# Performance work log

Hardware: AMD Instinct MI355X
Metric: run time of the kernel (lower is better)

The kernel has to match this reference:

```python
import jax, jax.numpy as jnp
import numpy as np

H, W, D = 160, 160, 16
VOXEL_SIZE = 0.4
VOL_MIN = np.array([-32.0, -32.0, -1.0], dtype=np.float32)
SCALE_MULTIPLIER = 3.0
N_GAUSS = 8192
CHUNK = 64


def setup_inputs() -> dict:
    key = jax.random.key(0)
    k1, k2, k3, k4, k5 = jax.random.split(key, 5)
    vol_min = jnp.asarray(VOL_MIN)
    vol_ext = jnp.array([64.0, 64.0, 6.4], dtype=jnp.float32)
    means3d = jax.random.uniform(k1, (N_GAUSS, 3), jnp.float32) * vol_ext + vol_min
    opacities = jax.random.uniform(k2, (N_GAUSS, 1), jnp.float32)
    # per-axis std devs: 0.2..0.8 m so 3-sigma footprint spans a handful of voxels
    scales = 0.2 + 0.6 * jax.random.uniform(k3, (N_GAUSS, 3), jnp.float32)
    rotations = jax.random.normal(k4, (N_GAUSS, 4), jnp.float32)
    features = jax.random.normal(k5, (N_GAUSS, 32), jnp.float32)
    return {"means3d": means3d, "opacities": opacities, "scales": scales,
            "rotations": rotations, "features": features}


def quat_to_rotmat(q):
    # q: [N,4] wxyz, normalized
    w, x, y, z = q[:, 0], q[:, 1], q[:, 2], q[:, 3]
    R = jnp.stack([
        jnp.stack([1 - 2 * (y * y + z * z), 2 * (x * y - w * z), 2 * (x * z + w * y)], -1),
        jnp.stack([2 * (x * y + w * z), 1 - 2 * (x * x + z * z), 2 * (y * z - w * x)], -1),
        jnp.stack([2 * (x * z - w * y), 2 * (y * z + w * x), 1 - 2 * (x * x + y * y)], -1),
    ], axis=-2)  # [N,3,3]
    return R


def _grid_coords():
    ii, jj, kk = jnp.meshgrid(jnp.arange(H), jnp.arange(W), jnp.arange(D), indexing="ij")
    idx = jnp.stack([ii, jj, kk], axis=-1).astype(jnp.float32)
    return (idx + 0.5) * VOXEL_SIZE + jnp.asarray(VOL_MIN)  # [H,W,D,3] voxel centers


def reference(means3d, opacities, scales, rotations, features):
    x = _grid_coords().reshape(-1, 3)  # [V,3]
    q = rotations / jnp.linalg.norm(rotations, axis=-1, keepdims=True)
    R = quat_to_rotmat(q)
    # covariance = R diag(s^2) R^T
    cov = jnp.einsum("nij,nj,nkj->nik", R, scales * scales, R)
    cov_inv = jnp.linalg.inv(cov)
    sigma = jnp.sqrt(jnp.diagonal(cov, axis1=1, axis2=2))  # [N,3]
    opac = opacities[:, 0]  # [N]
    n = means3d.shape[0]
    nchunks = n // CHUNK

    def chunked(a):
        return a.reshape(nchunks, CHUNK, *a.shape[1:])

    def step(acc, c):
        mu, op, sg, ci, ft = c
        diff = x[:, None, :] - mu[None, :, :]  # [V,CHUNK,3]
        maha = jnp.einsum("vci,cij,vcj->vc", diff, ci, diff)
        # local aggregation cutoff: within scale_multiplier * sigma box around mean
        mask = jnp.all(jnp.abs(diff) <= SCALE_MULTIPLIER * sg[None, :, :], axis=-1)
        w = op[None, :] * jnp.exp(-0.5 * maha) * mask  # [V,CHUNK]
        return acc + w @ ft, None

    acc0 = jnp.zeros((x.shape[0], features.shape[-1]), jnp.float32)
    xs = (chunked(means3d), chunked(opac), chunked(sigma), chunked(cov_inv), chunked(features))
    acc, _ = jax.lax.scan(step, acc0, xs)
    return acc.reshape(H, W, D, features.shape[-1])
```

## Files before the change

### kernel.cpp

```cpp
#include <hip/hip_runtime.h>

#define HH 160
#define WW 160
#define DD 16
#define NG 8192
#define VOXEL 0.4f

#define TTX 20
#define TTY 20
#define TTZ 4
#define NTILES (TTX * TTY * TTZ)
#define CAP 256


__global__ __launch_bounds__(256) void gv_precompute_bin(
    const float* __restrict__ means, const float* __restrict__ opac,
    const float* __restrict__ scales, const float* __restrict__ rots,
    float4* __restrict__ pack, int* __restrict__ tileCnt,
    int* __restrict__ tileList) {
  int g = blockIdx.x * 256 + threadIdx.x;
  if (g >= NG) return;
  float qw = rots[g * 4 + 0], qx = rots[g * 4 + 1];
  float qy = rots[g * 4 + 2], qz = rots[g * 4 + 3];
  float inv = rsqrtf(qw * qw + qx * qx + qy * qy + qz * qz);
  qw *= inv; qx *= inv; qy *= inv; qz *= inv;
  float R[3][3];
  R[0][0] = 1.f - 2.f * (qy * qy + qz * qz);
  R[0][1] = 2.f * (qx * qy - qw * qz);
  R[0][2] = 2.f * (qx * qz + qw * qy);
  R[1][0] = 2.f * (qx * qy + qw * qz);
  R[1][1] = 1.f - 2.f * (qx * qx + qz * qz);
  R[1][2] = 2.f * (qy * qz - qw * qx);
  R[2][0] = 2.f * (qx * qz - qw * qy);
  R[2][1] = 2.f * (qy * qz + qw * qx);
  R[2][2] = 1.f - 2.f * (qx * qx + qy * qy);
  float sx = scales[g * 3 + 0], sy = scales[g * 3 + 1], sz = scales[g * 3 + 2];
  float s2[3] = {sx * sx, sy * sy, sz * sz};
  float is2[3] = {1.f / s2[0], 1.f / s2[1], 1.f / s2[2]};
  float cov00 = 0.f, cov11 = 0.f, cov22 = 0.f;
  float ci00 = 0.f, ci01 = 0.f, ci02 = 0.f, ci11 = 0.f, ci12 = 0.f, ci22 = 0.f;
#pragma unroll
  for (int c = 0; c < 3; c++) {
    cov00 += R[0][c] * R[0][c] * s2[c];
    cov11 += R[1][c] * R[1][c] * s2[c];
    cov22 += R[2][c] * R[2][c] * s2[c];
    ci00 += R[0][c] * R[0][c] * is2[c];
    ci01 += R[0][c] * R[1][c] * is2[c];
    ci02 += R[0][c] * R[2][c] * is2[c];
    ci11 += R[1][c] * R[1][c] * is2[c];
    ci12 += R[1][c] * R[2][c] * is2[c];
    ci22 += R[2][c] * R[2][c] * is2[c];
  }
  float mx = means[g * 3 + 0], my = means[g * 3 + 1], mz = means[g * 3 + 2];
  float bx = 3.f * sqrtf(cov00), by = 3.f * sqrtf(cov11), bz = 3.f * sqrtf(cov22);
  float4* p = pack + (size_t)g * 4;
  p[0] = make_float4(mx, my, mz, opac[g]);
  p[1] = make_float4(bx, by, bz, ci00);
  p[2] = make_float4(ci01, ci02, ci11, ci12);
  p[3] = make_float4(ci22, 0.f, 0.f, 0.f);

  const float eps = 1e-4f;
  int i0 = (int)ceilf((mx - bx + 32.f) * 2.5f - 0.5f - eps);
  int i1 = (int)floorf((mx + bx + 32.f) * 2.5f - 0.5f + eps);
  int j0 = (int)ceilf((my - by + 32.f) * 2.5f - 0.5f - eps);
  int j1 = (int)floorf((my + by + 32.f) * 2.5f - 0.5f + eps);
  int k0 = (int)ceilf((mz - bz + 1.f) * 2.5f - 0.5f - eps);
  int k1 = (int)floorf((mz + bz + 1.f) * 2.5f - 0.5f + eps);
  i0 = max(i0, 0); i1 = min(i1, HH - 1);
  j0 = max(j0, 0); j1 = min(j1, WW - 1);
  k0 = max(k0, 0); k1 = min(k1, DD - 1);
  if (i0 > i1 || j0 > j1 || k0 > k1) return;
  int ti0 = i0 >> 3, ti1 = i1 >> 3;
  int tj0 = j0 >> 3, tj1 = j1 >> 3;
  int tk0 = k0 >> 2, tk1 = k1 >> 2;
  for (int ti = ti0; ti <= ti1; ti++)
    for (int tj = tj0; tj <= tj1; tj++)
      for (int tk = tk0; tk <= tk1; tk++) {
        int t = (ti * TTY + tj) * TTZ + tk;
        int pos = atomicAdd(&tileCnt[t], 1);
        if (pos < CAP) tileList[t * CAP + pos] = g;
      }
}

__global__ __launch_bounds__(256) void gv_voxelize(
    const float4* __restrict__ pack, const float4* __restrict__ feats,
    const int* __restrict__ tileCnt, const int* __restrict__ tileList,
    float4* __restrict__ out) {
  int tid = threadIdx.x;
  int dk = tid & 3, dj = (tid >> 2) & 7, di = tid >> 5;
  int tk = blockIdx.x, tj = blockIdx.y, ti = blockIdx.z;
  int i = ti * 8 + di, j = tj * 8 + dj, k = tk * 4 + dk;

  float px = (i + 0.5f) * VOXEL - 32.f;
  float py = (j + 0.5f) * VOXEL - 32.f;
  float pz = (k + 0.5f) * VOXEL - 1.f;

  int t = (ti * TTY + tj) * TTZ + tk;
  int cnt = tileCnt[t];
  cnt = min(cnt, CAP);
  const int* __restrict__ lst = tileList + t * CAP;

  float4 acc[8];
#pragma unroll
  for (int f = 0; f < 8; f++) acc[f] = make_float4(0.f, 0.f, 0.f, 0.f);

  for (int n = 0; n < cnt; n++) {
    int gg = __builtin_amdgcn_readfirstlane(lst[n]);
    const float4* __restrict__ p = pack + (size_t)gg * 4;
    float4 pa = p[0];
    float4 pb = p[1];
    float dx = px - pa.x, dy = py - pa.y, dz = pz - pa.z;
    bool in = (fabsf(dx) <= pb.x) & (fabsf(dy) <= pb.y) & (fabsf(dz) <= pb.z);
    if (__any(in)) {
      float4 pc = p[2];
      float4 pd = p[3];
      float maha = pb.w * dx * dx + pc.z * dy * dy + pd.x * dz * dz +
                   2.f * (pc.x * dx * dy + pc.y * dx * dz + pc.w * dy * dz);
      float w = in ? pa.w * __expf(-0.5f * maha) : 0.f;
      const float4* __restrict__ fp = feats + (size_t)gg * 8;
#pragma unroll
      for (int f = 0; f < 8; f++) {
        float4 fv = fp[f];
        acc[f].x += w * fv.x;
        acc[f].y += w * fv.y;
        acc[f].z += w * fv.z;
        acc[f].w += w * fv.w;
      }
    }
  }

  size_t v = ((size_t)i * WW + j) * DD + k;
  float4* o = out + v * 8;
#pragma unroll
  for (int f = 0; f < 8; f++) o[f] = acc[f];
}

extern "C" void kernel_launch(void* const* d_in, const int* in_sizes, int n_in,
                              void* d_out, int out_size, void* d_ws, size_t ws_size,
                              hipStream_t stream) {
  const float* means  = (const float*)d_in[0];
  const float* opac   = (const float*)d_in[1];
  const float* scales = (const float*)d_in[2];
  const float* rots   = (const float*)d_in[3];
  const float4* feats = (const float4*)d_in[4];

  char* ws = (char*)d_ws;
  float4* pack   = (float4*)ws;
  int* tileCnt   = (int*)(ws + 512 * 1024);
  int* tileList  = (int*)(ws + 520 * 1024);

  hipMemsetAsync(tileCnt, 0, NTILES * sizeof(int), stream);
  gv_precompute_bin<<<32, 256, 0, stream>>>(means, opac, scales, rots,
                                            pack, tileCnt, tileList);
  dim3 grid(TTZ, TTY, TTX);
  gv_voxelize<<<grid, 256, 0, stream>>>(pack, feats, tileCnt, tileList,
                                        (float4*)d_out);
}
```

Before: 139.9 us.

## Software-pipeline gaussian loads in voxelize loop and shrink bin kernel blocks

The voxelize loop now loads 64 tile-list entries at once into lanes, broadcasts each index with a shuffle, and double-buffers the packed gaussian parameters and features so the next gaussian's loads are in flight while the current one is computed. The aim is to hide global-load latency that was exposed in the serial loop. Features are now loaded unconditionally, even when no lane is inside the box, and the extra register buffers raise register pressure. The precompute/bin kernel is relaunched as 128 blocks of 64 threads to spread its work over more CUs.

Result: slower. 209.7 us (+49.9%).

```diff
diff --git a/kernel.cpp b/kernel.cpp
--- a/kernel.cpp
+++ b/kernel.cpp
@@ -13,12 +13,12 @@
 #define CAP 256
 
 
-__global__ __launch_bounds__(256) void gv_precompute_bin(
+__global__ __launch_bounds__(64) void gv_precompute_bin(
     const float* __restrict__ means, const float* __restrict__ opac,
     const float* __restrict__ scales, const float* __restrict__ rots,
     float4* __restrict__ pack, int* __restrict__ tileCnt,
     int* __restrict__ tileList) {
-  int g = blockIdx.x * 256 + threadIdx.x;
+  int g = blockIdx.x * 64 + threadIdx.x;
   if (g >= NG) return;
   float qw = rots[g * 4 + 0], qx = rots[g * 4 + 1];
   float qy = rots[g * 4 + 2], qz = rots[g * 4 + 3];
@@ -82,11 +82,41 @@
       }
 }
 
+#define LOADST(Pa, Pb, Pc, Pd, Pf, gg)                     \
+  do {                                                     \
+    const float4* _p = pack + (size_t)(gg) * 4;            \
+    Pa = _p[0]; Pb = _p[1]; Pc = _p[2]; Pd = _p[3];        \
+    const float4* _f = feats + (size_t)(gg) * 8;           \
+    _Pragma("unroll")                                      \
+    for (int f = 0; f < 8; f++) Pf[f] = _f[f];             \
+  } while (0)
+
+#define COMPUTE(Pa, Pb, Pc, Pd, Pf)                                       \
+  do {                                                                    \
+    float dx = px - Pa.x, dy = py - Pa.y, dz = pz - Pa.z;                 \
+    bool in = (fabsf(dx) <= Pb.x) & (fabsf(dy) <= Pb.y) &                 \
+              (fabsf(dz) <= Pb.z);                                        \
+    if (__any(in)) {                                                      \
+      float maha = Pb.w * dx * dx + Pc.z * dy * dy + Pd.x * dz * dz +     \
+                   2.f * (Pc.x * dx * dy + Pc.y * dx * dz +               \
+                          Pc.w * dy * dz);                                \
+      float wgt = in ? Pa.w * __expf(-0.5f * maha) : 0.f;                 \
+      _Pragma("unroll")                                                   \
+      for (int f = 0; f < 8; f++) {                                       \
+        acc[f].x += wgt * Pf[f].x;                                        \
+        acc[f].y += wgt * Pf[f].y;                                        \
+        acc[f].z += wgt * Pf[f].z;                                        \
+        acc[f].w += wgt * Pf[f].w;                                        \
+      }                                                                   \
+    }                                                                     \
+  } while (0)
+
 __global__ __launch_bounds__(256) void gv_voxelize(
     const float4* __restrict__ pack, const float4* __restrict__ feats,
     const int* __restrict__ tileCnt, const int* __restrict__ tileList,
     float4* __restrict__ out) {
   int tid = threadIdx.x;
+  int lane = tid & 63;
   int dk = tid & 3, dj = (tid >> 2) & 7, di = tid >> 5;
   int tk = blockIdx.x, tj = blockIdx.y, ti = blockIdx.z;
   int i = ti * 8 + di, j = tj * 8 + dj, k = tk * 4 + dk;
@@ -104,29 +134,28 @@
 #pragma unroll
   for (int f = 0; f < 8; f++) acc[f] = make_float4(0.f, 0.f, 0.f, 0.f);
 
-  for (int n = 0; n < cnt; n++) {
-    int gg = __builtin_amdgcn_readfirstlane(lst[n]);
-    const float4* __restrict__ p = pack + (size_t)gg * 4;
-    float4 pa = p[0];
-    float4 pb = p[1];
-    float dx = px - pa.x, dy = py - pa.y, dz = pz - pa.z;
-    bool in = (fabsf(dx) <= pb.x) & (fabsf(dy) <= pb.y) & (fabsf(dz) <= pb.z);
-    if (__any(in)) {
-      float4 pc = p[2];
-      float4 pd = p[3];
-      float maha = pb.w * dx * dx + pc.z * dy * dy + pd.x * dz * dz +
-                   2.f * (pc.x * dx * dy + pc.y * dx * dz + pc.w * dy * dz);
-      float w = in ? pa.w * __expf(-0.5f * maha) : 0.f;
-      const float4* __restrict__ fp = feats + (size_t)gg * 8;
-#pragma unroll
-      for (int f = 0; f < 8; f++) {
-        float4 fv = fp[f];
-        acc[f].x += w * fv.x;
-        acc[f].y += w * fv.y;
-        acc[f].z += w * fv.z;
-        acc[f].w += w * fv.w;
+  for (int base = 0; base < cnt; base += 64) {
+    int lv = lst[base + lane];
+    int M = min(64, cnt - base);
+
+    float4 Aa, Ab, Ac, Ad, Af[8];
+    float4 Ba, Bb, Bc, Bd, Bf[8];
+
+    int gA = __shfl(lv, 0);
+    LOADST(Aa, Ab, Ac, Ad, Af, gA);
+
+    int nn = 0;
+    for (; nn + 2 <= M; nn += 2) {
+      int gB = __shfl(lv, nn + 1);
+      LOADST(Ba, Bb, Bc, Bd, Bf, gB);
+      COMPUTE(Aa, Ab, Ac, Ad, Af);
+      if (nn + 2 < M) {
+        int gA2 = __shfl(lv, nn + 2);
+        LOADST(Aa, Ab, Ac, Ad, Af, gA2);
       }
+      COMPUTE(Ba, Bb, Bc, Bd, Bf);
     }
+    if (nn < M) COMPUTE(Aa, Ab, Ac, Ad, Af);
   }
 
   size_t v = ((size_t)i * WW + j) * DD + k;
@@ -150,7 +179,7 @@
   int* tileList  = (int*)(ws + 520 * 1024);
 
   hipMemsetAsync(tileCnt, 0, NTILES * sizeof(int), stream);
-  gv_precompute_bin<<<32, 256, 0, stream>>>(means, opac, scales, rots,
+  gv_precompute_bin<<<128, 64, 0, stream>>>(means, opac, scales, rots,
                                             pack, tileCnt, tileList);
   dim3 grid(TTZ, TTY, TTX);
   gv_voxelize<<<grid, 256, 0, stream>>>(pack, feats, tileCnt, tileList,
```

## Split tile gaussian list across wave pairs with shared-memory reduction

Applied to the files above, without the earlier changes.

The voxelize kernel now uses 512 threads per tile. Each voxel gets two waves that take alternating gaussians from the tile list, and their partial sums are combined through shared memory before the write. The wavefront-level any() branch is removed: all parameters and features are loaded up front and computed without a branch, which exposes more memory-level parallelism. The cost is extra work for gaussians that miss the whole wave and a barrier plus LDS traffic. The precompute kernel is relaunched as 128 blocks of 64 threads to spread it across more CUs.

New measurement: 128.7 us. 1.09x faster.

```diff
diff --git a/kernel.cpp b/kernel.cpp
--- a/kernel.cpp
+++ b/kernel.cpp
@@ -13,12 +13,12 @@
 #define CAP 256
 
 
-__global__ __launch_bounds__(256) void gv_precompute_bin(
+__global__ __launch_bounds__(64) void gv_precompute_bin(
     const float* __restrict__ means, const float* __restrict__ opac,
     const float* __restrict__ scales, const float* __restrict__ rots,
     float4* __restrict__ pack, int* __restrict__ tileCnt,
     int* __restrict__ tileList) {
-  int g = blockIdx.x * 256 + threadIdx.x;
+  int g = blockIdx.x * 64 + threadIdx.x;
   if (g >= NG) return;
   float qw = rots[g * 4 + 0], qx = rots[g * 4 + 1];
   float qy = rots[g * 4 + 2], qz = rots[g * 4 + 3];
@@ -82,12 +82,20 @@
       }
 }
 
-__global__ __launch_bounds__(256) void gv_voxelize(
+__global__ __launch_bounds__(512) void gv_voxelize(
     const float4* __restrict__ pack, const float4* __restrict__ feats,
     const int* __restrict__ tileCnt, const int* __restrict__ tileList,
     float4* __restrict__ out) {
+  __shared__ float4 s_red[4][64][9];
+
   int tid = threadIdx.x;
-  int dk = tid & 3, dj = (tid >> 2) & 7, di = tid >> 5;
+  int wid = tid >> 6;
+  int pair = wid >> 1;
+  int h = wid & 1;
+  int l = tid & 63;
+  int di = (pair >> 1) * 4 + (l >> 4);
+  int dj = (pair & 1) * 4 + ((l >> 2) & 3);
+  int dk = l & 3;
   int tk = blockIdx.x, tj = blockIdx.y, ti = blockIdx.z;
   int i = ti * 8 + di, j = tj * 8 + dj, k = tk * 4 + dk;
 
@@ -104,35 +112,45 @@
 #pragma unroll
   for (int f = 0; f < 8; f++) acc[f] = make_float4(0.f, 0.f, 0.f, 0.f);
 
-  for (int n = 0; n < cnt; n++) {
+  for (int n = h; n < cnt; n += 2) {
     int gg = __builtin_amdgcn_readfirstlane(lst[n]);
     const float4* __restrict__ p = pack + (size_t)gg * 4;
-    float4 pa = p[0];
-    float4 pb = p[1];
+    const float4* __restrict__ fp = feats + (size_t)gg * 8;
+    float4 pa = p[0], pb = p[1], pc = p[2], pd = p[3];
+    float4 f0 = fp[0], f1 = fp[1], f2 = fp[2], f3 = fp[3];
+    float4 f4 = fp[4], f5 = fp[5], f6 = fp[6], f7 = fp[7];
+
     float dx = px - pa.x, dy = py - pa.y, dz = pz - pa.z;
     bool in = (fabsf(dx) <= pb.x) & (fabsf(dy) <= pb.y) & (fabsf(dz) <= pb.z);
-    if (__any(in)) {
-      float4 pc = p[2];
-      float4 pd = p[3];
-      float maha = pb.w * dx * dx + pc.z * dy * dy + pd.x * dz * dz +
-                   2.f * (pc.x * dx * dy + pc.y * dx * dz + pc.w * dy * dz);
-      float w = in ? pa.w * __expf(-0.5f * maha) : 0.f;
-      const float4* __restrict__ fp = feats + (size_t)gg * 8;
+    float maha = pb.w * dx * dx + pc.z * dy * dy + pd.x * dz * dz +
+                 2.f * (pc.x * dx * dy + pc.y * dx * dz + pc.w * dy * dz);
+    float wgt = in ? pa.w * __expf(-0.5f * maha) : 0.f;
+
+    acc[0].x += wgt * f0.x; acc[0].y += wgt * f0.y; acc[0].z += wgt * f0.z; acc[0].w += wgt * f0.w;
+    acc[1].x += wgt * f1.x; acc[1].y += wgt * f1.y; acc[1].z += wgt * f1.z; acc[1].w += wgt * f1.w;
+    acc[2].x += wgt * f2.x; acc[2].y += wgt * f2.y; acc[2].z += wgt * f2.z; acc[2].w += wgt * f2.w;
+    acc[3].x += wgt * f3.x; acc[3].y += wgt * f3.y; acc[3].z += wgt * f3.z; acc[3].w += wgt * f3.w;
+    acc[4].x += wgt * f4.x; acc[4].y += wgt * f4.y; acc[4].z += wgt * f4.z; acc[4].w += wgt * f4.w;
+    acc[5].x += wgt * f5.x; acc[5].y += wgt * f5.y; acc[5].z += wgt * f5.z; acc[5].w += wgt * f5.w;
+    acc[6].x += wgt * f6.x; acc[6].y += wgt * f6.y; acc[6].z += wgt * f6.z; acc[6].w += wgt * f6.w;
+    acc[7].x += wgt * f7.x; acc[7].y += wgt * f7.y; acc[7].z += wgt * f7.z; acc[7].w += wgt * f7.w;
+  }
+
+  if (h) {
 #pragma unroll
-      for (int f = 0; f < 8; f++) {
-        float4 fv = fp[f];
-        acc[f].x += w * fv.x;
-        acc[f].y += w * fv.y;
-        acc[f].z += w * fv.z;
-        acc[f].w += w * fv.w;
-      }
+    for (int f = 0; f < 8; f++) s_red[pair][l][f] = acc[f];
+  }
+  __syncthreads();
+  if (!h) {
+    size_t v = ((size_t)i * WW + j) * DD + k;
+    float4* o = out + v * 8;
+#pragma unroll
+    for (int f = 0; f < 8; f++) {
+      float4 r = s_red[pair][l][f];
+      o[f] = make_float4(acc[f].x + r.x, acc[f].y + r.y,
+                         acc[f].z + r.z, acc[f].w + r.w);
     }
   }
-
-  size_t v = ((size_t)i * WW + j) * DD + k;
-  float4* o = out + v * 8;
-#pragma unroll
-  for (int f = 0; f < 8; f++) o[f] = acc[f];
 }
 
 extern "C" void kernel_launch(void* const* d_in, const int* in_sizes, int n_in,
@@ -150,9 +168,9 @@
   int* tileList  = (int*)(ws + 520 * 1024);
 
   hipMemsetAsync(tileCnt, 0, NTILES * sizeof(int), stream);
-  gv_precompute_bin<<<32, 256, 0, stream>>>(means, opac, scales, rots,
+  gv_precompute_bin<<<128, 64, 0, stream>>>(means, opac, scales, rots,
                                             pack, tileCnt, tileList);
   dim3 grid(TTZ, TTY, TTX);
-  gv_voxelize<<<grid, 256, 0, stream>>>(pack, feats, tileCnt, tileList,
+  gv_voxelize<<<grid, 512, 0, stream>>>(pack, feats, tileCnt, tileList,
                                         (float4*)d_out);
 }
```

## Store Gaussian params per tile and cull per wave with ballot

Applied to the files above, without the earlier changes.

Binning now writes the full packed Gaussian parameters directly into per-tile SoA slots instead of index lists, so the voxelize kernel loads 64 entries at once coalesced and broadcasts them via shuffles. Each wave pre-culls entries against its own 2x8x4 sub-box bounds using a ballot, then processes only surviving Gaussians, two at a time, to overlap feature loads. Tile capacity drops from 256 to 128 and the bin kernel uses 64-thread blocks. The smaller capacity risks silently dropping Gaussians in dense tiles, and the per-tile copies increase workspace writes.

Result: faster. 132.0 us (-5.7%).

```diff
diff --git a/kernel.cpp b/kernel.cpp
--- a/kernel.cpp
+++ b/kernel.cpp
@@ -10,15 +10,15 @@
 #define TTY 20
 #define TTZ 4
 #define NTILES (TTX * TTY * TTZ)
-#define CAP 256
-
-
-__global__ __launch_bounds__(256) void gv_precompute_bin(
+#define CAP 128
+#define PSTRIDE (NTILES * CAP)
+
+
+__global__ __launch_bounds__(64) void gv_precompute_bin(
     const float* __restrict__ means, const float* __restrict__ opac,
     const float* __restrict__ scales, const float* __restrict__ rots,
-    float4* __restrict__ pack, int* __restrict__ tileCnt,
-    int* __restrict__ tileList) {
-  int g = blockIdx.x * 256 + threadIdx.x;
+    int* __restrict__ tileCnt, float4* __restrict__ tilePack) {
+  int g = blockIdx.x * 64 + threadIdx.x;
   if (g >= NG) return;
   float qw = rots[g * 4 + 0], qx = rots[g * 4 + 1];
   float qy = rots[g * 4 + 2], qz = rots[g * 4 + 3];
@@ -53,11 +53,6 @@
   }
   float mx = means[g * 3 + 0], my = means[g * 3 + 1], mz = means[g * 3 + 2];
   float bx = 3.f * sqrtf(cov00), by = 3.f * sqrtf(cov11), bz = 3.f * sqrtf(cov22);
-  float4* p = pack + (size_t)g * 4;
-  p[0] = make_float4(mx, my, mz, opac[g]);
-  p[1] = make_float4(bx, by, bz, ci00);
-  p[2] = make_float4(ci01, ci02, ci11, ci12);
-  p[3] = make_float4(ci22, 0.f, 0.f, 0.f);
 
   const float eps = 1e-4f;
   int i0 = (int)ceilf((mx - bx + 32.f) * 2.5f - 0.5f - eps);
@@ -70,6 +65,12 @@
   j0 = max(j0, 0); j1 = min(j1, WW - 1);
   k0 = max(k0, 0); k1 = min(k1, DD - 1);
   if (i0 > i1 || j0 > j1 || k0 > k1) return;
+
+  float4 p0 = make_float4(mx, my, mz, opac[g]);
+  float4 p1 = make_float4(bx, by, bz, __int_as_float(g));
+  float4 p2 = make_float4(ci00, ci01, ci02, ci11);
+  float4 p3 = make_float4(ci12, ci22, 0.f, 0.f);
+
   int ti0 = i0 >> 3, ti1 = i1 >> 3;
   int tj0 = j0 >> 3, tj1 = j1 >> 3;
   int tk0 = k0 >> 2, tk1 = k1 >> 2;
@@ -78,15 +79,22 @@
       for (int tk = tk0; tk <= tk1; tk++) {
         int t = (ti * TTY + tj) * TTZ + tk;
         int pos = atomicAdd(&tileCnt[t], 1);
-        if (pos < CAP) tileList[t * CAP + pos] = g;
+        if (pos < CAP) {
+          size_t row = (size_t)t * CAP + pos;
+          tilePack[row] = p0;
+          tilePack[PSTRIDE + row] = p1;
+          tilePack[2 * PSTRIDE + row] = p2;
+          tilePack[3 * PSTRIDE + row] = p3;
+        }
       }
 }
 
 __global__ __launch_bounds__(256) void gv_voxelize(
-    const float4* __restrict__ pack, const float4* __restrict__ feats,
-    const int* __restrict__ tileCnt, const int* __restrict__ tileList,
-    float4* __restrict__ out) {
+    const float4* __restrict__ feats, const int* __restrict__ tileCnt,
+    const float4* __restrict__ tilePack, float4* __restrict__ out) {
   int tid = threadIdx.x;
+  int lane = tid & 63;
+  int w = tid >> 6;
   int dk = tid & 3, dj = (tid >> 2) & 7, di = tid >> 5;
   int tk = blockIdx.x, tj = blockIdx.y, ti = blockIdx.z;
   int i = ti * 8 + di, j = tj * 8 + dj, k = tk * 4 + dk;
@@ -95,39 +103,77 @@
   float py = (j + 0.5f) * VOXEL - 32.f;
   float pz = (k + 0.5f) * VOXEL - 1.f;
 
+  const float SLK = 1e-5f;
+  float cxlo = (ti * 8 + 2 * w + 0.5f) * VOXEL - 32.f;
+  float cxhi = (ti * 8 + 2 * w + 1 + 0.5f) * VOXEL - 32.f;
+  float cylo = (tj * 8 + 0.5f) * VOXEL - 32.f;
+  float cyhi = (tj * 8 + 7 + 0.5f) * VOXEL - 32.f;
+  float czlo = (tk * 4 + 0.5f) * VOXEL - 1.f;
+  float czhi = (tk * 4 + 3 + 0.5f) * VOXEL - 1.f;
+
   int t = (ti * TTY + tj) * TTZ + tk;
   int cnt = tileCnt[t];
   cnt = min(cnt, CAP);
-  const int* __restrict__ lst = tileList + t * CAP;
 
   float4 acc[8];
 #pragma unroll
   for (int f = 0; f < 8; f++) acc[f] = make_float4(0.f, 0.f, 0.f, 0.f);
 
-  for (int n = 0; n < cnt; n++) {
-    int gg = __builtin_amdgcn_readfirstlane(lst[n]);
-    const float4* __restrict__ p = pack + (size_t)gg * 4;
-    float4 pa = p[0];
-    float4 pb = p[1];
-    float dx = px - pa.x, dy = py - pa.y, dz = pz - pa.z;
-    bool in = (fabsf(dx) <= pb.x) & (fabsf(dy) <= pb.y) & (fabsf(dz) <= pb.z);
-    if (__any(in)) {
-      float4 pc = p[2];
-      float4 pd = p[3];
-      float maha = pb.w * dx * dx + pc.z * dy * dy + pd.x * dz * dz +
-                   2.f * (pc.x * dx * dy + pc.y * dx * dz + pc.w * dy * dz);
-      float w = in ? pa.w * __expf(-0.5f * maha) : 0.f;
-      const float4* __restrict__ fp = feats + (size_t)gg * 8;
-#pragma unroll
-      for (int f = 0; f < 8; f++) {
-        float4 fv = fp[f];
-        acc[f].x += w * fv.x;
-        acc[f].y += w * fv.y;
-        acc[f].z += w * fv.z;
-        acc[f].w += w * fv.w;
+#define SURV_BODY(M)                                                          \
+  do {                                                                        \
+    int _idx = __builtin_amdgcn_readlane(__float_as_int(pk1.w), (M));         \
+    const float4* __restrict__ _fp = feats + (size_t)_idx * 8;                \
+    float4 F[8];                                                              \
+    _Pragma("unroll")                                                         \
+    for (int f = 0; f < 8; f++) F[f] = _fp[f];                                \
+    float mux = __shfl(pk0.x, (M)), muy = __shfl(pk0.y, (M));                 \
+    float muz = __shfl(pk0.z, (M)), op = __shfl(pk0.w, (M));                  \
+    float bbx = __shfl(pk1.x, (M)), bby = __shfl(pk1.y, (M));                 \
+    float bbz = __shfl(pk1.z, (M));                                           \
+    float q00 = __shfl(pk2.x, (M)), q01 = __shfl(pk2.y, (M));                 \
+    float q02 = __shfl(pk2.z, (M)), q11 = __shfl(pk2.w, (M));                 \
+    float q12 = __shfl(pk3.x, (M)), q22 = __shfl(pk3.y, (M));                 \
+    float dx = px - mux, dy = py - muy, dz = pz - muz;                        \
+    bool in = (fabsf(dx) <= bbx) & (fabsf(dy) <= bby) & (fabsf(dz) <= bbz);   \
+    float maha = q00 * dx * dx + q11 * dy * dy + q22 * dz * dz +              \
+                 2.f * (q01 * dx * dy + q02 * dx * dz + q12 * dy * dz);       \
+    float wgt = in ? op * __expf(-0.5f * maha) : 0.f;                         \
+    _Pragma("unroll")                                                         \
+    for (int f = 0; f < 8; f++) {                                             \
+      acc[f].x += wgt * F[f].x;                                               \
+      acc[f].y += wgt * F[f].y;                                               \
+      acc[f].z += wgt * F[f].z;                                               \
+      acc[f].w += wgt * F[f].w;                                               \
+    }                                                                         \
+  } while (0)
+
+  for (int base = 0; base < cnt; base += 64) {
+    int m = base + lane;
+    int mm = min(m, cnt - 1);
+    size_t row = (size_t)t * CAP + mm;
+    float4 pk0 = tilePack[row];
+    float4 pk1 = tilePack[PSTRIDE + row];
+    float4 pk2 = tilePack[2 * PSTRIDE + row];
+    float4 pk3 = tilePack[3 * PSTRIDE + row];
+
+    bool sv = (m < cnt) &
+              (pk0.x >= cxlo - pk1.x - SLK) & (pk0.x <= cxhi + pk1.x + SLK) &
+              (pk0.y >= cylo - pk1.y - SLK) & (pk0.y <= cyhi + pk1.y + SLK) &
+              (pk0.z >= czlo - pk1.z - SLK) & (pk0.z <= czhi + pk1.z + SLK);
+    unsigned long long mask = __ballot(sv);
+
+    while (mask) {
+      int m0 = __ffsll(mask) - 1; mask &= mask - 1;
+      if (mask) {
+        int m1 = __ffsll(mask) - 1; mask &= mask - 1;
+        SURV_BODY(m0);
+        SURV_BODY(m1);
+      } else {
+        SURV_BODY(m0);
       }
     }
   }
+#undef SURV_BODY
 
   size_t v = ((size_t)i * WW + j) * DD + k;
   float4* o = out + v * 8;
@@ -145,14 +191,13 @@
   const float4* feats = (const float4*)d_in[4];
 
   char* ws = (char*)d_ws;
-  float4* pack   = (float4*)ws;
-  int* tileCnt   = (int*)(ws + 512 * 1024);
-  int* tileList  = (int*)(ws + 520 * 1024);
+  int* tileCnt     = (int*)ws;
+  float4* tilePack = (float4*)(ws + 64 * 1024);
 
   hipMemsetAsync(tileCnt, 0, NTILES * sizeof(int), stream);
-  gv_precompute_bin<<<32, 256, 0, stream>>>(means, opac, scales, rots,
-                                            pack, tileCnt, tileList);
+  gv_precompute_bin<<<128, 64, 0, stream>>>(means, opac, scales, rots,
+                                            tileCnt, tilePack);
   dim3 grid(TTZ, TTY, TTX);
-  gv_voxelize<<<grid, 256, 0, stream>>>(pack, feats, tileCnt, tileList,
+  gv_voxelize<<<grid, 256, 0, stream>>>(feats, tileCnt, tilePack,
                                         (float4*)d_out);
 }
```
